# Kernel tuning notes

Hardware: AMD Instinct MI355X
Metric: run time of the kernel (lower is better)

## Reference

```python
import jax, jax.numpy as jnp
import numpy as np

N_EMBD = 2048
HEAD_SIZE = 128

def setup_inputs() -> dict:
    key = jax.random.key(0)
    kx, kk, kq, kv = jax.random.split(key, 4)
    bound = 1.0 / np.sqrt(N_EMBD)  # torch Linear default init range
    x = jax.random.normal(kx, (4, 4096, N_EMBD), dtype=jnp.float32)
    Wk = jax.random.uniform(kk, (N_EMBD, HEAD_SIZE), jnp.float32, -bound, bound)
    Wq = jax.random.uniform(kq, (N_EMBD, HEAD_SIZE), jnp.float32, -bound, bound)
    Wv = jax.random.uniform(kv, (N_EMBD, HEAD_SIZE), jnp.float32, -bound, bound)
    return {"x": x, "Wk": Wk, "Wq": Wq, "Wv": Wv}

def reference(x, Wk, Wq, Wv):
    B, T, C = x.shape
    k = jnp.einsum('btc,ch->bth', x, Wk)
    q = jnp.einsum('btc,ch->bth', x, Wq)
    v = jnp.einsum('btc,ch->bth', x, Wv)
    # NOTE: original scales by C**-0.5 where C = n_embd (input dim), not head_size
    scores = jnp.einsum('bth,bsh->bts', q, k) * (C ** -0.5)
    causal = jnp.tril(jnp.ones((T, T), dtype=bool))  # [T,T]
    scores = jnp.where(causal, scores, -jnp.inf)
    probs = jax.nn.softmax(scores, axis=-1)
    # dropout_probability = 0.0 -> identity
    return jnp.einsum('bts,bsh->bth', probs, v)
```

## Files before the change

kernel.cpp:

```cpp
#include <hip/hip_runtime.h>
#include <hip/hip_bf16.h>

#define T_SEQ 4096
#define NB 4
#define CEMB 2048
#define HS 128

typedef __attribute__((ext_vector_type(8))) short bf16x8;
typedef __attribute__((ext_vector_type(4))) float f32x4;
typedef __attribute__((ext_vector_type(16))) float f32x16;

__device__ inline short f2bf(float f) {
    union { float f; unsigned u; } v; v.f = f;
    unsigned r = v.u + 0x7FFFu + ((v.u >> 16) & 1u);
    return (short)(r >> 16);
}

__device__ inline unsigned pk2(float lo, float hi) {
    unsigned r;
    asm("v_cvt_pk_bf16_f32 %0, %1, %2" : "=v"(r) : "v"(lo), "v"(hi));
    return r;
}

__device__ inline void gld16(const void* gsrc, void* lds) {
    __builtin_amdgcn_global_load_lds(
        (const __attribute__((address_space(1))) unsigned*)gsrc,
        (__attribute__((address_space(3))) unsigned*)lds, 16, 0, 0);
}

__global__ __launch_bounds__(256) void wt_kernel(
    const float* __restrict__ Wq, const float* __restrict__ Wk,
    const float* __restrict__ Wv, short* __restrict__ Wt) {
    int d = blockIdx.x * 256 + threadIdx.x;
    int mat = d >> 18;
    int rm  = d & 262143;
    int s   = rm >> 13;
    int e   = rm & 8191;
    int p   = e * 2;
    int n   = p >> 7;
    int lin = p ^ ((n & 7) << 4);
    int kk  = (lin & 127) >> 1;
    int k   = s * 64 + kk;
    const float* W = (mat == 0) ? Wq : (mat == 1) ? Wk : Wv;
    Wt[d] = f2bf(W[k * HS + n]);
}

__global__ __launch_bounds__(256, 3) void proj_kernel(
    const float* __restrict__ x, const short* __restrict__ Wt,
    short* __restrict__ qg, short* __restrict__ kg, short* __restrict__ vtg) {
    __shared__ short Wlds[3][8192];

    const int tid = threadIdx.x;
    const int w   = tid >> 6;
    const int l   = tid & 63;
    const int lg  = l >> 4;
    const int lr  = l & 15;

    const int bid = blockIdx.x;
    const int wk  = (bid & 7) * 96 + (bid >> 3);
    const int mat = wk % 3;
    const int m0  = (wk / 3) * 64;

    const short* Wp = Wt + (long)mat * 262144;

    f32x4 acc[8];
    #pragma unroll
    for (int b = 0; b < 8; b++) acc[b] = (f32x4){0.f, 0.f, 0.f, 0.f};

    const float* xrow = x + (long)(m0 + w * 16 + lr) * CEMB;
    const int sw = (lr & 7) << 4;

    float4 xs[3][4];

#define STAGE(S, B) do {                                                   \
        const short* gp_ = Wp + (long)(S) * 8192 + (long)(w * 4) * 512 + l * 8; \
        gld16(gp_,        &Wlds[B][(w * 4 + 0) * 512]);                    \
        gld16(gp_ + 512,  &Wlds[B][(w * 4 + 1) * 512]);                    \
        gld16(gp_ + 1024, &Wlds[B][(w * 4 + 2) * 512]);                    \
        gld16(gp_ + 1536, &Wlds[B][(w * 4 + 3) * 512]);                    \
    } while (0)

#define LOADX(S, B) do {                                                   \
        const float* xn_ = xrow + (S) * 64;                                \
        xs[B][0] = *reinterpret_cast<const float4*>(xn_ + lg * 8);         \
        xs[B][1] = *reinterpret_cast<const float4*>(xn_ + lg * 8 + 4);     \
        xs[B][2] = *reinterpret_cast<const float4*>(xn_ + 32 + lg * 8);    \
        xs[B][3] = *reinterpret_cast<const float4*>(xn_ + 32 + lg * 8 + 4);\
    } while (0)

    STAGE(0, 0);
    LOADX(0, 0);
    STAGE(1, 1);
    LOADX(1, 1);

#define STEP(S, B0, B2) do {                                               \
        asm volatile("s_waitcnt vmcnt(8) lgkmcnt(0)\n\ts_barrier" ::: "memory"); \
        if ((S) + 2 < 32) { STAGE((S) + 2, B2); LOADX((S) + 2, B2); }      \
        bf16x8 a0, a1;                                                     \
        a0[0] = f2bf(xs[B0][0].x); a0[1] = f2bf(xs[B0][0].y);              \
        a0[2] = f2bf(xs[B0][0].z); a0[3] = f2bf(xs[B0][0].w);              \
        a0[4] = f2bf(xs[B0][1].x); a0[5] = f2bf(xs[B0][1].y);              \
        a0[6] = f2bf(xs[B0][1].z); a0[7] = f2bf(xs[B0][1].w);              \
        a1[0] = f2bf(xs[B0][2].x); a1[1] = f2bf(xs[B0][2].y);              \
        a1[2] = f2bf(xs[B0][2].z); a1[3] = f2bf(xs[B0][2].w);              \
        a1[4] = f2bf(xs[B0][3].x); a1[5] = f2bf(xs[B0][3].y);              \
        a1[6] = f2bf(xs[B0][3].z); a1[7] = f2bf(xs[B0][3].w);              \
        const char* lbase_ = (const char*)&Wlds[B0][0];                    \
        _Pragma("unroll")                                                  \
        for (int nt = 0; nt < 8; nt++) {                                   \
            int off_ = (((nt * 16 + lr) * 128 + lg * 16)) ^ sw;            \
            bf16x8 bfr_ = *reinterpret_cast<const bf16x8*>(lbase_ + off_); \
            acc[nt] = __builtin_amdgcn_mfma_f32_16x16x32_bf16(             \
                a0, bfr_, acc[nt], 0, 0, 0);                               \
        }                                                                  \
        _Pragma("unroll")                                                  \
        for (int nt = 0; nt < 8; nt++) {                                   \
            int off_ = (((nt * 16 + lr) * 128 + lg * 16 + 64)) ^ sw;       \
            bf16x8 bfr_ = *reinterpret_cast<const bf16x8*>(lbase_ + off_); \
            acc[nt] = __builtin_amdgcn_mfma_f32_16x16x32_bf16(             \
                a1, bfr_, acc[nt], 0, 0, 0);                               \
        }                                                                  \
    } while (0)

    for (int s = 0; s < 30; s += 3) {
        STEP(s, 0, 2);
        STEP(s + 1, 1, 0);
        STEP(s + 2, 2, 1);
    }
    STEP(30, 0, 2);
    STEP(31, 1, 0);

#undef STEP
#undef LOADX
#undef STAGE

    if (mat == 0) {
        const float scale = 0.0318793851f;
        #pragma unroll
        for (int nt = 0; nt < 8; nt++)
            #pragma unroll
            for (int r = 0; r < 4; r++) {
                int row = m0 + w * 16 + lg * 4 + r;
                qg[(long)row * HS + nt * 16 + lr] = f2bf(acc[nt][r] * scale);
            }
    } else if (mat == 1) {
        short* kt = kg + ((long)(m0 >> 6)) * 8192;
        #pragma unroll
        for (int nt = 0; nt < 8; nt++)
            #pragma unroll
            for (int r = 0; r < 4; r++) {
                int r64  = w * 16 + lg * 4 + r;
                int byte = (r64 * 256 + (nt * 16 + lr) * 2) ^ ((r64 & 7) << 4);
                kt[byte >> 1] = f2bf(acc[nt][r]);
            }
    } else {
        #pragma unroll
        for (int nt = 0; nt < 8; nt++)
            #pragma unroll
            for (int r = 0; r < 4; r++) {
                int row = m0 + w * 16 + lg * 4 + r;
                int b   = row >> 12;
                int tl  = row & 4095;
                vtg[(long)b * (HS * T_SEQ) + (long)(nt * 16 + lr) * T_SEQ + tl]
                    = f2bf(acc[nt][r]);
            }
    }
}

__global__ __launch_bounds__(512, 2) void attn_kernel(
    const short* __restrict__ qg, const short* __restrict__ kg,
    const short* __restrict__ vtg, float* __restrict__ out) {
    __shared__ __align__(16) char pool[131072];
    __shared__ float Lm[8][32];
    __shared__ float Ll[8][32];

    const int tid = threadIdx.x;
    const int w   = tid >> 6;
    const int l   = tid & 63;
    const int c31 = l & 31;
    const int hi  = l >> 5;
    const int hi4 = hi << 2;
    const int hi8 = hi << 3;

    const int bid = blockIdx.x;
    const int xcd = bid & 7;
    const int idx = bid >> 3;
    const int b   = xcd >> 1;
    const int qtA = 127 - ((idx << 1) | (xcd & 1));

    const short* kbimg = kg + (long)b * 64 * 8192;
    const short* vb    = vtg + (long)b * HS * T_SEQ;

    short* Kw = (short*)(pool + (w << 14));

#define STAGEK(TILE) do {                                                  \
        const short* gp_ = kbimg + (long)(TILE) * 8192 + l * 8;            \
        _Pragma("unroll")                                                  \
        for (int i = 0; i < 16; i++)                                       \
            gld16(gp_ + i * 512, Kw + i * 512 + l * 8);                    \
    } while (0)

    const int swz = (c31 & 7) << 4;
    const int rbA = c31 * 256;
    const int rbB = (32 + c31) * 256;

    #pragma unroll 1
    for (int ph = 0; ph < 2; ++ph) {
        const int qt   = ph ? (127 - qtA) : qtA;
        const int q0   = qt * 32;
        const int qrow = q0 + c31;
        const int ntk  = (qt >> 1) + 1;

        bf16x8 qf[8];
        #pragma unroll
        for (int kc = 0; kc < 8; kc++)
            qf[kc] = *reinterpret_cast<const bf16x8*>(
                &qg[(long)(b * T_SEQ + qrow) * HS + kc * 16 + hi8]);

        f32x16 accO[4];
        #pragma unroll
        for (int nb = 0; nb < 4; nb++)
            #pragma unroll
            for (int i = 0; i < 16; i++) accO[nb][i] = 0.f;
        float mrow = -__builtin_inff();
        float lsum = 0.f;

        if (w < ntk) STAGEK(w);

        #pragma unroll 1
        for (int t = w; t < ntk; t += 8) {
            const int kv0 = t * 64;

            asm volatile("s_waitcnt vmcnt(0)" ::: "memory");

            bf16x8 vfA[2][4];
            #pragma unroll
            for (int kc = 0; kc < 2; kc++)
                #pragma unroll
                for (int nb = 0; nb < 4; nb++)
                    vfA[kc][nb] = *reinterpret_cast<const bf16x8*>(
                        &vb[(long)(nb * 32 + c31) * T_SEQ + kv0 + kc * 16 + hi8]);

            f32x16 SA, SB;
            #pragma unroll
            for (int i = 0; i < 16; i++) { SA[i] = 0.f; SB[i] = 0.f; }
            __builtin_amdgcn_s_setprio(1);
            #pragma unroll
            for (int kc = 0; kc < 8; kc++) {
                const int cb = kc * 32 + hi * 16;
                bf16x8 ka = *reinterpret_cast<const bf16x8*>(
                    (const char*)Kw + ((rbA + cb) ^ swz));
                bf16x8 kb2 = *reinterpret_cast<const bf16x8*>(
                    (const char*)Kw + ((rbB + cb) ^ swz));
                SA = __builtin_amdgcn_mfma_f32_32x32x16_bf16(ka,  qf[kc], SA, 0, 0, 0);
                SB = __builtin_amdgcn_mfma_f32_32x32x16_bf16(kb2, qf[kc], SB, 0, 0, 0);
            }
            __builtin_amdgcn_s_setprio(0);

            if (t + 8 < ntk) STAGEK(t + 8);

            float pA[16], pB[16];
            #pragma unroll
            for (int r = 0; r < 16; r++) { pA[r] = SA[r]; pB[r] = SB[r]; }

            if (kv0 + 63 > q0) {
                #pragma unroll
                for (int r = 0; r < 16; r++) {
                    int kr = kv0 + (r & 3) + 8 * (r >> 2) + hi4;
                    pA[r] = (kr > qrow)      ? -__builtin_inff() : pA[r];
                    pB[r] = (kr + 32 > qrow) ? -__builtin_inff() : pB[r];
                }
            }

            float t16[16];
            #pragma unroll
            for (int r = 0; r < 16; r++) t16[r] = fmaxf(pA[r], pB[r]);
            #pragma unroll
            for (int s2 = 8; s2 >= 1; s2 >>= 1)
                #pragma unroll
                for (int r = 0; r < 8; r++)
                    if (r < s2) t16[r] = fmaxf(t16[r], t16[r + s2]);
            float mt = fmaxf(t16[0], __shfl_xor(t16[0], 32));

            if (__any(mt > mrow)) {
                float mnew = fmaxf(mrow, mt);
                float fac  = exp2f(mrow - mnew);
                lsum *= fac;
                #pragma unroll
                for (int nb = 0; nb < 4; nb++)
                    #pragma unroll
                    for (int i = 0; i < 16; i++) accO[nb][i] *= fac;
                mrow = mnew;
            }

            bf16x8 vfB[2][4];
            #pragma unroll
            for (int kc = 0; kc < 2; kc++)
                #pragma unroll
                for (int nb = 0; nb < 4; nb++)
                    vfB[kc][nb] = *reinterpret_cast<const bf16x8*>(
                        &vb[(long)(nb * 32 + c31) * T_SEQ + kv0 + (kc + 2) * 16 + hi8]);

            #pragma unroll
            for (int r = 0; r < 16; r++) {
                pA[r] = exp2f(pA[r] - mrow);
                pB[r] = exp2f(pB[r] - mrow);
            }
            float s16[16];
            #pragma unroll
            for (int r = 0; r < 16; r++) s16[r] = pA[r] + pB[r];
            #pragma unroll
            for (int s2 = 8; s2 >= 1; s2 >>= 1)
                #pragma unroll
                for (int r = 0; r < 8; r++)
                    if (r < s2) s16[r] += s16[r + s2];
            lsum += s16[0] + __shfl_xor(s16[0], 32);

            bf16x8 pf[4];
            #pragma unroll
            for (int kc = 0; kc < 4; kc++) {
                const int V0 = 2 * kc, V1 = 2 * kc + 1;
                const int r0 = ((V0 >> 2) << 4) | ((V0 & 3) << 2);
                const int r1 = ((V1 >> 2) << 4) | ((V1 & 3) << 2);
#define PSEL(i) ((i) < 16 ? pA[(i) & 15] : pB[(i) & 15])
                unsigned a0 = pk2(PSEL(r0 + 0), PSEL(r0 + 1));
                unsigned a1 = pk2(PSEL(r0 + 2), PSEL(r0 + 3));
                unsigned b0 = pk2(PSEL(r1 + 0), PSEL(r1 + 1));
                unsigned b1 = pk2(PSEL(r1 + 2), PSEL(r1 + 3));
#undef PSEL
                unsigned k0 = hi ? b0 : a0, k1 = hi ? b1 : a1;
                unsigned s0 = hi ? a0 : b0, s1 = hi ? a1 : b1;
                unsigned g0 = (unsigned)__shfl_xor((int)s0, 32);
                unsigned g1 = (unsigned)__shfl_xor((int)s1, 32);
                union { unsigned u[4]; bf16x8 v; } U;
                U.u[0] = hi ? g0 : k0;
                U.u[1] = hi ? g1 : k1;
                U.u[2] = hi ? k0 : g0;
                U.u[3] = hi ? k1 : g1;
                pf[kc] = U.v;
            }

            __builtin_amdgcn_s_setprio(1);
            #pragma unroll
            for (int nb = 0; nb < 4; nb++)
                accO[nb] = __builtin_amdgcn_mfma_f32_32x32x16_bf16(pf[0], vfA[0][nb], accO[nb], 0, 0, 0);
            #pragma unroll
            for (int nb = 0; nb < 4; nb++)
                accO[nb] = __builtin_amdgcn_mfma_f32_32x32x16_bf16(pf[1], vfA[1][nb], accO[nb], 0, 0, 0);
            #pragma unroll
            for (int nb = 0; nb < 4; nb++)
                accO[nb] = __builtin_amdgcn_mfma_f32_32x32x16_bf16(pf[2], vfB[0][nb], accO[nb], 0, 0, 0);
            #pragma unroll
            for (int nb = 0; nb < 4; nb++)
                accO[nb] = __builtin_amdgcn_mfma_f32_32x32x16_bf16(pf[3], vfB[1][nb], accO[nb], 0, 0, 0);
            __builtin_amdgcn_s_setprio(0);
        }

        __syncthreads();
        {
            float* LaccW = (float*)(pool + (w << 14));
            #pragma unroll
            for (int nb = 0; nb < 4; nb++)
                #pragma unroll
                for (int r = 0; r < 16; r++)
                    LaccW[((r & 3) + 8 * (r >> 2) + hi4) * 128 + nb * 32 + c31] = accO[nb][r];
            if (l < 32) { Lm[w][c31] = mrow; Ll[w][c31] = lsum; }
        }
        __syncthreads();

        {
            const int row = tid >> 4;
            const int c0  = (tid & 15) * 8;
            float mv[8], lv[8];
            #pragma unroll
            for (int p2 = 0; p2 < 8; p2++) { mv[p2] = Lm[p2][row]; lv[p2] = Ll[p2][row]; }
            float ms = mv[0];
            #pragma unroll
            for (int p2 = 1; p2 < 8; p2++) ms = fmaxf(ms, mv[p2]);
            float fv[8];
            float L = 0.f;
            #pragma unroll
            for (int p2 = 0; p2 < 8; p2++) { fv[p2] = exp2f(mv[p2] - ms); L += lv[p2] * fv[p2]; }
            float inv = 1.0f / L;
            float* op = &out[((long)b * T_SEQ + q0 + row) * HS + c0];
            #pragma unroll
            for (int j = 0; j < 8; j++) {
                float o = 0.f;
                #pragma unroll
                for (int p2 = 0; p2 < 8; p2++)
                    o += ((const float*)(pool + (p2 << 14)))[row * 128 + c0 + j] * fv[p2];
                op[j] = o * inv;
            }
        }
        __syncthreads();
    }
#undef STAGEK
}

extern "C" void kernel_launch(void* const* d_in, const int* in_sizes, int n_in,
                              void* d_out, int out_size, void* d_ws, size_t ws_size,
                              hipStream_t stream) {
    const float* x  = (const float*)d_in[0];
    const float* Wk = (const float*)d_in[1];
    const float* Wq = (const float*)d_in[2];
    const float* Wv = (const float*)d_in[3];
    float* out = (float*)d_out;

    char* ws = (char*)d_ws;
    short* Wt  = (short*)ws;
    short* qg  = (short*)(ws + 1572864);
    short* kg  = (short*)(ws + 1572864 + 4194304);
    short* vtg = (short*)(ws + 1572864 + 8388608);

    wt_kernel  <<<3072, 256, 0, stream>>>(Wq, Wk, Wv, Wt);
    proj_kernel<<<768,  256, 0, stream>>>(x, Wt, qg, kg, vtg);
    attn_kernel<<<256,  512, 0, stream>>>(qg, kg, vtg, out);
}
```

Baseline: 133.5 us.

## Double projection block rows to 128 with 8 waves sharing each weight stage

The projection kernel now uses 512-thread blocks that each cover 128 rows instead of 64, so every weight tile staged in LDS serves twice as many rows and weight traffic per row is halved. The x prefetch becomes single-buffered: x is converted to bf16 right after the barrier and the next slice is loaded immediately, which cuts register use (launch bounds now ask for 6 waves per SIMD). The key-tile store indexing is adjusted for the larger block. In exchange, the loop is no longer unrolled, x load latency is hidden behind only one step of MFMA work, and there are half as many blocks to fill the CUs.

```diff
diff --git a/kernel.cpp b/kernel.cpp
--- a/kernel.cpp
+++ b/kernel.cpp
@@ -45,7 +45,7 @@
     Wt[d] = f2bf(W[k * HS + n]);
 }
 
-__global__ __launch_bounds__(256, 3) void proj_kernel(
+__global__ __launch_bounds__(512, 6) void proj_kernel(
     const float* __restrict__ x, const short* __restrict__ Wt,
     short* __restrict__ qg, short* __restrict__ kg, short* __restrict__ vtg) {
     __shared__ short Wlds[3][8192];
@@ -57,9 +57,9 @@
     const int lr  = l & 15;
 
     const int bid = blockIdx.x;
-    const int wk  = (bid & 7) * 96 + (bid >> 3);
+    const int wk  = (bid & 7) * 48 + (bid >> 3);
     const int mat = wk % 3;
-    const int m0  = (wk / 3) * 64;
+    const int m0  = (wk / 3) * 128;
 
     const short* Wp = Wt + (long)mat * 262144;
 
@@ -70,67 +70,74 @@
     const float* xrow = x + (long)(m0 + w * 16 + lr) * CEMB;
     const int sw = (lr & 7) << 4;
 
-    float4 xs[3][4];
+    float4 xs0, xs1, xs2, xs3;
 
 #define STAGE(S, B) do {                                                   \
-        const short* gp_ = Wp + (long)(S) * 8192 + (long)(w * 4) * 512 + l * 8; \
-        gld16(gp_,        &Wlds[B][(w * 4 + 0) * 512]);                    \
-        gld16(gp_ + 512,  &Wlds[B][(w * 4 + 1) * 512]);                    \
-        gld16(gp_ + 1024, &Wlds[B][(w * 4 + 2) * 512]);                    \
-        gld16(gp_ + 1536, &Wlds[B][(w * 4 + 3) * 512]);                    \
+        const short* gp_ = Wp + (long)(S) * 8192 + (long)(w * 2) * 512 + l * 8; \
+        gld16(gp_,       &Wlds[B][(w * 2 + 0) * 512]);                     \
+        gld16(gp_ + 512, &Wlds[B][(w * 2 + 1) * 512]);                     \
     } while (0)
 
-#define LOADX(S, B) do {                                                   \
+#define LOADX(S) do {                                                      \
         const float* xn_ = xrow + (S) * 64;                                \
-        xs[B][0] = *reinterpret_cast<const float4*>(xn_ + lg * 8);         \
-        xs[B][1] = *reinterpret_cast<const float4*>(xn_ + lg * 8 + 4);     \
-        xs[B][2] = *reinterpret_cast<const float4*>(xn_ + 32 + lg * 8);    \
-        xs[B][3] = *reinterpret_cast<const float4*>(xn_ + 32 + lg * 8 + 4);\
+        xs0 = *reinterpret_cast<const float4*>(xn_ + lg * 8);              \
+        xs1 = *reinterpret_cast<const float4*>(xn_ + lg * 8 + 4);          \
+        xs2 = *reinterpret_cast<const float4*>(xn_ + 32 + lg * 8);         \
+        xs3 = *reinterpret_cast<const float4*>(xn_ + 32 + lg * 8 + 4);     \
     } while (0)
 
-    STAGE(0, 0);
-    LOADX(0, 0);
-    STAGE(1, 1);
-    LOADX(1, 1);
-
-#define STEP(S, B0, B2) do {                                               \
-        asm volatile("s_waitcnt vmcnt(8) lgkmcnt(0)\n\ts_barrier" ::: "memory"); \
-        if ((S) + 2 < 32) { STAGE((S) + 2, B2); LOADX((S) + 2, B2); }      \
-        bf16x8 a0, a1;                                                     \
-        a0[0] = f2bf(xs[B0][0].x); a0[1] = f2bf(xs[B0][0].y);              \
-        a0[2] = f2bf(xs[B0][0].z); a0[3] = f2bf(xs[B0][0].w);              \
-        a0[4] = f2bf(xs[B0][1].x); a0[5] = f2bf(xs[B0][1].y);              \
-        a0[6] = f2bf(xs[B0][1].z); a0[7] = f2bf(xs[B0][1].w);              \
-        a1[0] = f2bf(xs[B0][2].x); a1[1] = f2bf(xs[B0][2].y);              \
-        a1[2] = f2bf(xs[B0][2].z); a1[3] = f2bf(xs[B0][2].w);              \
-        a1[4] = f2bf(xs[B0][3].x); a1[5] = f2bf(xs[B0][3].y);              \
-        a1[6] = f2bf(xs[B0][3].z); a1[7] = f2bf(xs[B0][3].w);              \
-        const char* lbase_ = (const char*)&Wlds[B0][0];                    \
+#define CONVERT(A0, A1) do {                                               \
+        A0[0] = f2bf(xs0.x); A0[1] = f2bf(xs0.y);                          \
+        A0[2] = f2bf(xs0.z); A0[3] = f2bf(xs0.w);                          \
+        A0[4] = f2bf(xs1.x); A0[5] = f2bf(xs1.y);                          \
+        A0[6] = f2bf(xs1.z); A0[7] = f2bf(xs1.w);                          \
+        A1[0] = f2bf(xs2.x); A1[1] = f2bf(xs2.y);                          \
+        A1[2] = f2bf(xs2.z); A1[3] = f2bf(xs2.w);                          \
+        A1[4] = f2bf(xs3.x); A1[5] = f2bf(xs3.y);                          \
+        A1[6] = f2bf(xs3.z); A1[7] = f2bf(xs3.w);                          \
+    } while (0)
+
+#define MFMA16(LB) do {                                                    \
         _Pragma("unroll")                                                  \
         for (int nt = 0; nt < 8; nt++) {                                   \
             int off_ = (((nt * 16 + lr) * 128 + lg * 16)) ^ sw;            \
-            bf16x8 bfr_ = *reinterpret_cast<const bf16x8*>(lbase_ + off_); \
+            bf16x8 bfr_ = *reinterpret_cast<const bf16x8*>((LB) + off_);   \
             acc[nt] = __builtin_amdgcn_mfma_f32_16x16x32_bf16(             \
                 a0, bfr_, acc[nt], 0, 0, 0);                               \
         }                                                                  \
         _Pragma("unroll")                                                  \
         for (int nt = 0; nt < 8; nt++) {                                   \
             int off_ = (((nt * 16 + lr) * 128 + lg * 16 + 64)) ^ sw;       \
-            bf16x8 bfr_ = *reinterpret_cast<const bf16x8*>(lbase_ + off_); \
+            bf16x8 bfr_ = *reinterpret_cast<const bf16x8*>((LB) + off_);   \
             acc[nt] = __builtin_amdgcn_mfma_f32_16x16x32_bf16(             \
                 a1, bfr_, acc[nt], 0, 0, 0);                               \
         }                                                                  \
     } while (0)
 
-    for (int s = 0; s < 30; s += 3) {
-        STEP(s, 0, 2);
-        STEP(s + 1, 1, 0);
-        STEP(s + 2, 2, 1);
+    LOADX(0);
+    STAGE(0, 0);
+    STAGE(1, 1);
+
+    #pragma unroll 1
+    for (int s = 0; s < 31; ++s) {
+        asm volatile("s_waitcnt vmcnt(2) lgkmcnt(0)\n\ts_barrier" ::: "memory");
+        bf16x8 a0, a1;
+        CONVERT(a0, a1);
+        LOADX(s + 1);
+        if (s + 2 < 32) STAGE(s + 2, (s + 2) % 3);
+        const char* lbase_ = (const char*)&Wlds[s % 3][0];
+        MFMA16(lbase_);
     }
-    STEP(30, 0, 2);
-    STEP(31, 1, 0);
-
-#undef STEP
+    {
+        asm volatile("s_waitcnt vmcnt(0) lgkmcnt(0)\n\ts_barrier" ::: "memory");
+        bf16x8 a0, a1;
+        CONVERT(a0, a1);
+        const char* lbase_ = (const char*)&Wlds[31 % 3][0];
+        MFMA16(lbase_);
+    }
+
+#undef MFMA16
+#undef CONVERT
 #undef LOADX
 #undef STAGE
 
@@ -144,14 +151,15 @@
                 qg[(long)row * HS + nt * 16 + lr] = f2bf(acc[nt][r] * scale);
             }
     } else if (mat == 1) {
-        short* kt = kg + ((long)(m0 >> 6)) * 8192;
         #pragma unroll
         for (int nt = 0; nt < 8; nt++)
             #pragma unroll
             for (int r = 0; r < 4; r++) {
-                int r64  = w * 16 + lg * 4 + r;
+                int gr   = w * 16 + lg * 4 + r;
+                long tile = (m0 >> 6) + (gr >> 6);
+                int r64  = gr & 63;
                 int byte = (r64 * 256 + (nt * 16 + lr) * 2) ^ ((r64 & 7) << 4);
-                kt[byte >> 1] = f2bf(acc[nt][r]);
+                kg[tile * 8192 + (byte >> 1)] = f2bf(acc[nt][r]);
             }
     } else {
         #pragma unroll
@@ -413,6 +421,6 @@
     short* vtg = (short*)(ws + 1572864 + 8388608);
 
     wt_kernel  <<<3072, 256, 0, stream>>>(Wq, Wk, Wv, Wt);
-    proj_kernel<<<768,  256, 0, stream>>>(x, Wt, qg, kg, vtg);
+    proj_kernel<<<384,  512, 0, stream>>>(x, Wt, qg, kg, vtg);
     attn_kernel<<<256,  512, 0, stream>>>(qg, kg, vtg, out);
 }
```

After: 169.3 us. +26.9%, slower.

## Rewrite projection GEMM with 32x32 MFMA and direct fragment-layout weight loads

Applied to the files above, without the earlier changes.

The projection kernel drops its LDS-staged, barrier-synchronised triple-buffered weight pipeline. Weights are now pre-permuted into the per-lane fragment layout of 32x32x16 MFMA and read straight from global/L2 into registers, and x rows are software-prefetched one step ahead. Each wave computes a 32x64 tile instead of 16x128, and bf16 conversion uses the packed cvt instruction. This removes LDS traffic and block barriers, at the cost of more global weight reads per wave that rely on cache hits.

```diff
diff --git a/kernel.cpp b/kernel.cpp
--- a/kernel.cpp
+++ b/kernel.cpp
@@ -31,139 +31,113 @@
 __global__ __launch_bounds__(256) void wt_kernel(
     const float* __restrict__ Wq, const float* __restrict__ Wk,
     const float* __restrict__ Wv, short* __restrict__ Wt) {
-    int d = blockIdx.x * 256 + threadIdx.x;
-    int mat = d >> 18;
-    int rm  = d & 262143;
-    int s   = rm >> 13;
-    int e   = rm & 8191;
-    int p   = e * 2;
-    int n   = p >> 7;
-    int lin = p ^ ((n & 7) << 4);
-    int kk  = (lin & 127) >> 1;
-    int k   = s * 64 + kk;
+    int idx = blockIdx.x * 256 + threadIdx.x;
+    int j    = idx & 7;
+    int lane = (idx >> 3) & 63;
+    int c32  = (idx >> 9) & 3;
+    int k16  = (idx >> 11) & 127;
+    int mat  = idx >> 18;
+    int col  = c32 * 32 + (lane & 31);
+    int k    = k16 * 16 + ((lane >> 5) << 3) + j;
     const float* W = (mat == 0) ? Wq : (mat == 1) ? Wk : Wv;
-    Wt[d] = f2bf(W[k * HS + n]);
+    Wt[idx] = f2bf(W[k * HS + col]);
 }
 
 __global__ __launch_bounds__(256, 3) void proj_kernel(
     const float* __restrict__ x, const short* __restrict__ Wt,
     short* __restrict__ qg, short* __restrict__ kg, short* __restrict__ vtg) {
-    __shared__ short Wlds[3][8192];
-
     const int tid = threadIdx.x;
     const int w   = tid >> 6;
     const int l   = tid & 63;
-    const int lg  = l >> 4;
-    const int lr  = l & 15;
+    const int c31 = l & 31;
+    const int hi  = l >> 5;
 
     const int bid = blockIdx.x;
     const int wk  = (bid & 7) * 96 + (bid >> 3);
     const int mat = wk % 3;
     const int m0  = (wk / 3) * 64;
 
-    const short* Wp = Wt + (long)mat * 262144;
-
-    f32x4 acc[8];
+    const int rgbase = (w >> 1) << 5;
+    const int wc     = (w & 1) << 6;
+    const int c32b   = wc >> 5;
+
+    const short* Wm = Wt + (long)mat * 262144;
+    const float* xrow = x + (long)(m0 + rgbase + c31) * CEMB + hi * 8;
+
+    f32x16 acc0, acc1;
     #pragma unroll
-    for (int b = 0; b < 8; b++) acc[b] = (f32x4){0.f, 0.f, 0.f, 0.f};
-
-    const float* xrow = x + (long)(m0 + w * 16 + lr) * CEMB;
-    const int sw = (lr & 7) << 4;
-
-    float4 xs[3][4];
-
-#define STAGE(S, B) do {                                                   \
-        const short* gp_ = Wp + (long)(S) * 8192 + (long)(w * 4) * 512 + l * 8; \
-        gld16(gp_,        &Wlds[B][(w * 4 + 0) * 512]);                    \
-        gld16(gp_ + 512,  &Wlds[B][(w * 4 + 1) * 512]);                    \
-        gld16(gp_ + 1024, &Wlds[B][(w * 4 + 2) * 512]);                    \
-        gld16(gp_ + 1536, &Wlds[B][(w * 4 + 3) * 512]);                    \
-    } while (0)
-
-#define LOADX(S, B) do {                                                   \
-        const float* xn_ = xrow + (S) * 64;                                \
-        xs[B][0] = *reinterpret_cast<const float4*>(xn_ + lg * 8);         \
-        xs[B][1] = *reinterpret_cast<const float4*>(xn_ + lg * 8 + 4);     \
-        xs[B][2] = *reinterpret_cast<const float4*>(xn_ + 32 + lg * 8);    \
-        xs[B][3] = *reinterpret_cast<const float4*>(xn_ + 32 + lg * 8 + 4);\
-    } while (0)
-
-    STAGE(0, 0);
-    LOADX(0, 0);
-    STAGE(1, 1);
-    LOADX(1, 1);
-
-#define STEP(S, B0, B2) do {                                               \
-        asm volatile("s_waitcnt vmcnt(8) lgkmcnt(0)\n\ts_barrier" ::: "memory"); \
-        if ((S) + 2 < 32) { STAGE((S) + 2, B2); LOADX((S) + 2, B2); }      \
-        bf16x8 a0, a1;                                                     \
-        a0[0] = f2bf(xs[B0][0].x); a0[1] = f2bf(xs[B0][0].y);              \
-        a0[2] = f2bf(xs[B0][0].z); a0[3] = f2bf(xs[B0][0].w);              \
-        a0[4] = f2bf(xs[B0][1].x); a0[5] = f2bf(xs[B0][1].y);              \
-        a0[6] = f2bf(xs[B0][1].z); a0[7] = f2bf(xs[B0][1].w);              \
-        a1[0] = f2bf(xs[B0][2].x); a1[1] = f2bf(xs[B0][2].y);              \
-        a1[2] = f2bf(xs[B0][2].z); a1[3] = f2bf(xs[B0][2].w);              \
-        a1[4] = f2bf(xs[B0][3].x); a1[5] = f2bf(xs[B0][3].y);              \
-        a1[6] = f2bf(xs[B0][3].z); a1[7] = f2bf(xs[B0][3].w);              \
-        const char* lbase_ = (const char*)&Wlds[B0][0];                    \
-        _Pragma("unroll")                                                  \
-        for (int nt = 0; nt < 8; nt++) {                                   \
-            int off_ = (((nt * 16 + lr) * 128 + lg * 16)) ^ sw;            \
-            bf16x8 bfr_ = *reinterpret_cast<const bf16x8*>(lbase_ + off_); \
-            acc[nt] = __builtin_amdgcn_mfma_f32_16x16x32_bf16(             \
-                a0, bfr_, acc[nt], 0, 0, 0);                               \
-        }                                                                  \
-        _Pragma("unroll")                                                  \
-        for (int nt = 0; nt < 8; nt++) {                                   \
-            int off_ = (((nt * 16 + lr) * 128 + lg * 16 + 64)) ^ sw;       \
-            bf16x8 bfr_ = *reinterpret_cast<const bf16x8*>(lbase_ + off_); \
-            acc[nt] = __builtin_amdgcn_mfma_f32_16x16x32_bf16(             \
-                a1, bfr_, acc[nt], 0, 0, 0);                               \
-        }                                                                  \
-    } while (0)
-
-    for (int s = 0; s < 30; s += 3) {
-        STEP(s, 0, 2);
-        STEP(s + 1, 1, 0);
-        STEP(s + 2, 2, 1);
+    for (int i = 0; i < 16; i++) { acc0[i] = 0.f; acc1[i] = 0.f; }
+
+    float4 xc[4][2], xn[4][2];
+    #pragma unroll
+    for (int kc = 0; kc < 4; kc++) {
+        xc[kc][0] = *reinterpret_cast<const float4*>(xrow + kc * 16);
+        xc[kc][1] = *reinterpret_cast<const float4*>(xrow + kc * 16 + 4);
     }
-    STEP(30, 0, 2);
-    STEP(31, 1, 0);
-
-#undef STEP
-#undef LOADX
-#undef STAGE
+
+    #pragma unroll 2
+    for (int s = 0; s < 32; ++s) {
+        if (s < 31) {
+            const float* xp = xrow + (s + 1) * 64;
+            #pragma unroll
+            for (int kc = 0; kc < 4; kc++) {
+                xn[kc][0] = *reinterpret_cast<const float4*>(xp + kc * 16);
+                xn[kc][1] = *reinterpret_cast<const float4*>(xp + kc * 16 + 4);
+            }
+        }
+
+        #pragma unroll
+        for (int kc = 0; kc < 4; kc++) {
+            union { unsigned u[4]; bf16x8 v; } A;
+            A.u[0] = pk2(xc[kc][0].x, xc[kc][0].y);
+            A.u[1] = pk2(xc[kc][0].z, xc[kc][0].w);
+            A.u[2] = pk2(xc[kc][1].x, xc[kc][1].y);
+            A.u[3] = pk2(xc[kc][1].z, xc[kc][1].w);
+
+            const long k16 = (long)(s * 4 + kc);
+            bf16x8 w0 = *reinterpret_cast<const bf16x8*>(
+                Wm + (k16 * 4 + c32b) * 512 + l * 8);
+            bf16x8 w1 = *reinterpret_cast<const bf16x8*>(
+                Wm + (k16 * 4 + c32b + 1) * 512 + l * 8);
+
+            acc0 = __builtin_amdgcn_mfma_f32_32x32x16_bf16(A.v, w0, acc0, 0, 0, 0);
+            acc1 = __builtin_amdgcn_mfma_f32_32x32x16_bf16(A.v, w1, acc1, 0, 0, 0);
+        }
+
+        #pragma unroll
+        for (int kc = 0; kc < 4; kc++) { xc[kc][0] = xn[kc][0]; xc[kc][1] = xn[kc][1]; }
+    }
 
     if (mat == 0) {
         const float scale = 0.0318793851f;
         #pragma unroll
-        for (int nt = 0; nt < 8; nt++)
-            #pragma unroll
-            for (int r = 0; r < 4; r++) {
-                int row = m0 + w * 16 + lg * 4 + r;
-                qg[(long)row * HS + nt * 16 + lr] = f2bf(acc[nt][r] * scale);
-            }
+        for (int r = 0; r < 16; r++) {
+            int grow = m0 + rgbase + (r & 3) + 8 * (r >> 2) + 4 * hi;
+            qg[(long)grow * HS + wc + c31]      = f2bf(acc0[r] * scale);
+            qg[(long)grow * HS + wc + 32 + c31] = f2bf(acc1[r] * scale);
+        }
     } else if (mat == 1) {
-        short* kt = kg + ((long)(m0 >> 6)) * 8192;
-        #pragma unroll
-        for (int nt = 0; nt < 8; nt++)
-            #pragma unroll
-            for (int r = 0; r < 4; r++) {
-                int r64  = w * 16 + lg * 4 + r;
-                int byte = (r64 * 256 + (nt * 16 + lr) * 2) ^ ((r64 & 7) << 4);
-                kt[byte >> 1] = f2bf(acc[nt][r]);
-            }
+        #pragma unroll
+        for (int r = 0; r < 16; r++) {
+            int grow = m0 + rgbase + (r & 3) + 8 * (r >> 2) + 4 * hi;
+            long tile = grow >> 6;
+            int r64  = grow & 63;
+            int d0   = wc + c31;
+            int b0   = (r64 * 256 + d0 * 2) ^ ((r64 & 7) << 4);
+            int b1   = (r64 * 256 + (d0 + 32) * 2) ^ ((r64 & 7) << 4);
+            kg[tile * 8192 + (b0 >> 1)] = f2bf(acc0[r]);
+            kg[tile * 8192 + (b1 >> 1)] = f2bf(acc1[r]);
+        }
     } else {
         #pragma unroll
-        for (int nt = 0; nt < 8; nt++)
-            #pragma unroll
-            for (int r = 0; r < 4; r++) {
-                int row = m0 + w * 16 + lg * 4 + r;
-                int b   = row >> 12;
-                int tl  = row & 4095;
-                vtg[(long)b * (HS * T_SEQ) + (long)(nt * 16 + lr) * T_SEQ + tl]
-                    = f2bf(acc[nt][r]);
-            }
+        for (int r = 0; r < 16; r++) {
+            int grow = m0 + rgbase + (r & 3) + 8 * (r >> 2) + 4 * hi;
+            int b2 = grow >> 12;
+            int tl = grow & 4095;
+            int d0 = wc + c31;
+            vtg[(long)b2 * (HS * T_SEQ) + (long)d0 * T_SEQ + tl]        = f2bf(acc0[r]);
+            vtg[(long)b2 * (HS * T_SEQ) + (long)(d0 + 32) * T_SEQ + tl] = f2bf(acc1[r]);
+        }
     }
 }
 
```

Result: slower. 181.3 us (+35.8%).

## Repartition projection GEMM so each wave owns private W columns without barriers

Applied to the files above, without the earlier changes.

The projection kernel now gives each wave a private 32-column slice of the weight tile across all 64 rows, instead of splitting rows across waves that share the whole weight tile. Each wave then reads only its own LDS region, so the per-step workgroup barrier is removed and LDS shrinks to a double buffer. The weight pre-layout kernel is rewritten to match, and x-to-bf16 conversion switches to the packed hardware convert. The trade-off is that every wave now loads x for all 64 rows, which quadruples x global traffic per block, and the K-step is halved so there are twice as many iterations.

```diff
diff --git a/kernel.cpp b/kernel.cpp
--- a/kernel.cpp
+++ b/kernel.cpp
@@ -32,23 +32,22 @@
     const float* __restrict__ Wq, const float* __restrict__ Wk,
     const float* __restrict__ Wv, short* __restrict__ Wt) {
     int d = blockIdx.x * 256 + threadIdx.x;
+    int j   = d & 7;
+    int l   = (d >> 3) & 63;
+    int ct  = (d >> 9) & 1;
+    int wq  = (d >> 10) & 3;
+    int s2  = (d >> 12) & 63;
     int mat = d >> 18;
-    int rm  = d & 262143;
-    int s   = rm >> 13;
-    int e   = rm & 8191;
-    int p   = e * 2;
-    int n   = p >> 7;
-    int lin = p ^ ((n & 7) << 4);
-    int kk  = (lin & 127) >> 1;
-    int k   = s * 64 + kk;
+    int col = wq * 32 + ct * 16 + (l & 15);
+    int k   = s2 * 32 + ((l >> 4) << 3) + j;
     const float* W = (mat == 0) ? Wq : (mat == 1) ? Wk : Wv;
-    Wt[d] = f2bf(W[k * HS + n]);
+    Wt[d] = f2bf(W[k * HS + col]);
 }
 
 __global__ __launch_bounds__(256, 3) void proj_kernel(
     const float* __restrict__ x, const short* __restrict__ Wt,
     short* __restrict__ qg, short* __restrict__ kg, short* __restrict__ vtg) {
-    __shared__ short Wlds[3][8192];
+    __shared__ short Wlds[2][4][1024];
 
     const int tid = threadIdx.x;
     const int w   = tid >> 6;
@@ -61,74 +60,110 @@
     const int mat = wk % 3;
     const int m0  = (wk / 3) * 64;
 
-    const short* Wp = Wt + (long)mat * 262144;
-
-    f32x4 acc[8];
+    const short* Wp = Wt + (long)mat * 262144 + w * 1024;
+
+    f32x4 acc[4][2];
     #pragma unroll
-    for (int b = 0; b < 8; b++) acc[b] = (f32x4){0.f, 0.f, 0.f, 0.f};
-
-    const float* xrow = x + (long)(m0 + w * 16 + lr) * CEMB;
-    const int sw = (lr & 7) << 4;
-
-    float4 xs[3][4];
-
-#define STAGE(S, B) do {                                                   \
-        const short* gp_ = Wp + (long)(S) * 8192 + (long)(w * 4) * 512 + l * 8; \
-        gld16(gp_,        &Wlds[B][(w * 4 + 0) * 512]);                    \
-        gld16(gp_ + 512,  &Wlds[B][(w * 4 + 1) * 512]);                    \
-        gld16(gp_ + 1024, &Wlds[B][(w * 4 + 2) * 512]);                    \
-        gld16(gp_ + 1536, &Wlds[B][(w * 4 + 3) * 512]);                    \
+    for (int a = 0; a < 4; a++)
+        #pragma unroll
+        for (int b = 0; b < 2; b++) acc[a][b] = (f32x4){0.f, 0.f, 0.f, 0.f};
+
+    const float* xr0 = x + (long)(m0 + 0 * 16 + lr) * CEMB + lg * 8;
+    const float* xr1 = x + (long)(m0 + 1 * 16 + lr) * CEMB + lg * 8;
+    const float* xr2 = x + (long)(m0 + 2 * 16 + lr) * CEMB + lg * 8;
+    const float* xr3 = x + (long)(m0 + 3 * 16 + lr) * CEMB + lg * 8;
+
+    float4 xs[2][8];
+
+#define STAGE(S2, B) do {                                                  \
+        const short* gp_ = Wp + (long)(S2) * 4096 + l * 8;                 \
+        gld16(gp_,       &Wlds[B][w][0]);                                  \
+        gld16(gp_ + 512, &Wlds[B][w][512]);                                \
     } while (0)
 
-#define LOADX(S, B) do {                                                   \
-        const float* xn_ = xrow + (S) * 64;                                \
-        xs[B][0] = *reinterpret_cast<const float4*>(xn_ + lg * 8);         \
-        xs[B][1] = *reinterpret_cast<const float4*>(xn_ + lg * 8 + 4);     \
-        xs[B][2] = *reinterpret_cast<const float4*>(xn_ + 32 + lg * 8);    \
-        xs[B][3] = *reinterpret_cast<const float4*>(xn_ + 32 + lg * 8 + 4);\
+#define LOADX(S2, XB) do {                                                 \
+        xs[XB][0] = *reinterpret_cast<const float4*>(xr0 + (S2) * 32);     \
+        xs[XB][1] = *reinterpret_cast<const float4*>(xr0 + (S2) * 32 + 4); \
+        xs[XB][2] = *reinterpret_cast<const float4*>(xr1 + (S2) * 32);     \
+        xs[XB][3] = *reinterpret_cast<const float4*>(xr1 + (S2) * 32 + 4); \
+        xs[XB][4] = *reinterpret_cast<const float4*>(xr2 + (S2) * 32);     \
+        xs[XB][5] = *reinterpret_cast<const float4*>(xr2 + (S2) * 32 + 4); \
+        xs[XB][6] = *reinterpret_cast<const float4*>(xr3 + (S2) * 32);     \
+        xs[XB][7] = *reinterpret_cast<const float4*>(xr3 + (S2) * 32 + 4); \
     } while (0)
 
+#define STEP(S2) do {                                                      \
+        asm volatile("s_waitcnt vmcnt(8)" ::: "memory");                   \
+        if ((S2) + 1 < 64) {                                               \
+            STAGE((S2) + 1, ((S2) + 1) & 1);                               \
+            __builtin_amdgcn_sched_barrier(0);         \
+        }                                                                  \
+        const char* lb_ = (const char*)&Wlds[(S2) & 1][w][0] + l * 16;     \
+        bf16x8 b0_ = *reinterpret_cast<const bf16x8*>(lb_);                \
+        bf16x8 b1_ = *reinterpret_cast<const bf16x8*>(lb_ + 1024);        \
+        bf16x8 A0_, A1_, A2_, A3_;                                         \
+        {                                                                  \
+            union { unsigned u[4]; bf16x8 v; } U_;                         \
+            U_.u[0] = pk2(xs[(S2) & 1][0].x, xs[(S2) & 1][0].y);           \
+            U_.u[1] = pk2(xs[(S2) & 1][0].z, xs[(S2) & 1][0].w);           \
+            U_.u[2] = pk2(xs[(S2) & 1][1].x, xs[(S2) & 1][1].y);           \
+            U_.u[3] = pk2(xs[(S2) & 1][1].z, xs[(S2) & 1][1].w);           \
+            A0_ = U_.v;                                                    \
+            U_.u[0] = pk2(xs[(S2) & 1][2].x, xs[(S2) & 1][2].y);           \
+            U_.u[1] = pk2(xs[(S2) & 1][2].z, xs[(S2) & 1][2].w);           \
+            U_.u[2] = pk2(xs[(S2) & 1][3].x, xs[(S2) & 1][3].y);           \
+            U_.u[3] = pk2(xs[(S2) & 1][3].z, xs[(S2) & 1][3].w);           \
+            A1_ = U_.v;                                                    \
+            U_.u[0] = pk2(xs[(S2) & 1][4].x, xs[(S2) & 1][4].y);           \
+            U_.u[1] = pk2(xs[(S2) & 1][4].z, xs[(S2) & 1][4].w);           \
+            U_.u[2] = pk2(xs[(S2) & 1][5].x, xs[(S2) & 1][5].y);           \
+            U_.u[3] = pk2(xs[(S2) & 1][5].z, xs[(S2) & 1][5].w);           \
+            A2_ = U_.v;                                                    \
+            U_.u[0] = pk2(xs[(S2) & 1][6].x, xs[(S2) & 1][6].y);           \
+            U_.u[1] = pk2(xs[(S2) & 1][6].z, xs[(S2) & 1][6].w);           \
+            U_.u[2] = pk2(xs[(S2) & 1][7].x, xs[(S2) & 1][7].y);           \
+            U_.u[3] = pk2(xs[(S2) & 1][7].z, xs[(S2) & 1][7].w);           \
+            A3_ = U_.v;                                                    \
+        }                                                                  \
+        if ((S2) + 2 < 64) LOADX((S2) + 2, (S2) & 1);                      \
+        acc[0][0] = __builtin_amdgcn_mfma_f32_16x16x32_bf16(A0_, b0_, acc[0][0], 0, 0, 0); \
+        acc[0][1] = __builtin_amdgcn_mfma_f32_16x16x32_bf16(A0_, b1_, acc[0][1], 0, 0, 0); \
+        acc[1][0] = __builtin_amdgcn_mfma_f32_16x16x32_bf16(A1_, b0_, acc[1][0], 0, 0, 0); \
+        acc[1][1] = __builtin_amdgcn_mfma_f32_16x16x32_bf16(A1_, b1_, acc[1][1], 0, 0, 0); \
+        acc[2][0] = __builtin_amdgcn_mfma_f32_16x16x32_bf16(A2_, b0_, acc[2][0], 0, 0, 0); \
+        acc[2][1] = __builtin_amdgcn_mfma_f32_16x16x32_bf16(A2_, b1_, acc[2][1], 0, 0, 0); \
+        acc[3][0] = __builtin_amdgcn_mfma_f32_16x16x32_bf16(A3_, b0_, acc[3][0], 0, 0, 0); \
+        acc[3][1] = __builtin_amdgcn_mfma_f32_16x16x32_bf16(A3_, b1_, acc[3][1], 0, 0, 0); \
+    } while (0)
+
     STAGE(0, 0);
+    __builtin_amdgcn_sched_barrier(0);
     LOADX(0, 0);
-    STAGE(1, 1);
     LOADX(1, 1);
 
-#define STEP(S, B0, B2) do {                                               \
-        asm volatile("s_waitcnt vmcnt(8) lgkmcnt(0)\n\ts_barrier" ::: "memory"); \
-        if ((S) + 2 < 32) { STAGE((S) + 2, B2); LOADX((S) + 2, B2); }      \
-        bf16x8 a0, a1;                                                     \
-        a0[0] = f2bf(xs[B0][0].x); a0[1] = f2bf(xs[B0][0].y);              \
-        a0[2] = f2bf(xs[B0][0].z); a0[3] = f2bf(xs[B0][0].w);              \
-        a0[4] = f2bf(xs[B0][1].x); a0[5] = f2bf(xs[B0][1].y);              \
-        a0[6] = f2bf(xs[B0][1].z); a0[7] = f2bf(xs[B0][1].w);              \
-        a1[0] = f2bf(xs[B0][2].x); a1[1] = f2bf(xs[B0][2].y);              \
-        a1[2] = f2bf(xs[B0][2].z); a1[3] = f2bf(xs[B0][2].w);              \
-        a1[4] = f2bf(xs[B0][3].x); a1[5] = f2bf(xs[B0][3].y);              \
-        a1[6] = f2bf(xs[B0][3].z); a1[7] = f2bf(xs[B0][3].w);              \
-        const char* lbase_ = (const char*)&Wlds[B0][0];                    \
-        _Pragma("unroll")                                                  \
-        for (int nt = 0; nt < 8; nt++) {                                   \
-            int off_ = (((nt * 16 + lr) * 128 + lg * 16)) ^ sw;            \
-            bf16x8 bfr_ = *reinterpret_cast<const bf16x8*>(lbase_ + off_); \
-            acc[nt] = __builtin_amdgcn_mfma_f32_16x16x32_bf16(             \
-                a0, bfr_, acc[nt], 0, 0, 0);                               \
-        }                                                                  \
-        _Pragma("unroll")                                                  \
-        for (int nt = 0; nt < 8; nt++) {                                   \
-            int off_ = (((nt * 16 + lr) * 128 + lg * 16 + 64)) ^ sw;       \
-            bf16x8 bfr_ = *reinterpret_cast<const bf16x8*>(lbase_ + off_); \
-            acc[nt] = __builtin_amdgcn_mfma_f32_16x16x32_bf16(             \
-                a1, bfr_, acc[nt], 0, 0, 0);                               \
-        }                                                                  \
-    } while (0)
-
-    for (int s = 0; s < 30; s += 3) {
-        STEP(s, 0, 2);
-        STEP(s + 1, 1, 0);
-        STEP(s + 2, 2, 1);
+    #pragma unroll
+    for (int s2 = 0; s2 < 63; ++s2) STEP(s2);
+    {
+        asm volatile("s_waitcnt vmcnt(0)" ::: "memory");
+        const char* lb_ = (const char*)&Wlds[63 & 1][w][0] + l * 16;
+        bf16x8 b0_ = *reinterpret_cast<const bf16x8*>(lb_);
+        bf16x8 b1_ = *reinterpret_cast<const bf16x8*>(lb_ + 1024);
+        union { unsigned u[4]; bf16x8 v; } U_;
+        bf16x8 A_[4];
+        #pragma unroll
+        for (int rgp = 0; rgp < 4; rgp++) {
+            U_.u[0] = pk2(xs[1][rgp * 2].x, xs[1][rgp * 2].y);
+            U_.u[1] = pk2(xs[1][rgp * 2].z, xs[1][rgp * 2].w);
+            U_.u[2] = pk2(xs[1][rgp * 2 + 1].x, xs[1][rgp * 2 + 1].y);
+            U_.u[3] = pk2(xs[1][rgp * 2 + 1].z, xs[1][rgp * 2 + 1].w);
+            A_[rgp] = U_.v;
+        }
+        #pragma unroll
+        for (int rgp = 0; rgp < 4; rgp++) {
+            acc[rgp][0] = __builtin_amdgcn_mfma_f32_16x16x32_bf16(A_[rgp], b0_, acc[rgp][0], 0, 0, 0);
+            acc[rgp][1] = __builtin_amdgcn_mfma_f32_16x16x32_bf16(A_[rgp], b1_, acc[rgp][1], 0, 0, 0);
+        }
     }
-    STEP(30, 0, 2);
-    STEP(31, 1, 0);
 
 #undef STEP
 #undef LOADX
@@ -137,33 +172,42 @@
     if (mat == 0) {
         const float scale = 0.0318793851f;
         #pragma unroll
-        for (int nt = 0; nt < 8; nt++)
-            #pragma unroll
-            for (int r = 0; r < 4; r++) {
-                int row = m0 + w * 16 + lg * 4 + r;
-                qg[(long)row * HS + nt * 16 + lr] = f2bf(acc[nt][r] * scale);
-            }
+        for (int rgp = 0; rgp < 4; rgp++)
+            #pragma unroll
+            for (int ct = 0; ct < 2; ct++)
+                #pragma unroll
+                for (int r = 0; r < 4; r++) {
+                    int row = m0 + rgp * 16 + lg * 4 + r;
+                    int col = w * 32 + ct * 16 + lr;
+                    qg[(long)row * HS + col] = f2bf(acc[rgp][ct][r] * scale);
+                }
     } else if (mat == 1) {
         short* kt = kg + ((long)(m0 >> 6)) * 8192;
         #pragma unroll
-        for (int nt = 0; nt < 8; nt++)
-            #pragma unroll
-            for (int r = 0; r < 4; r++) {
-                int r64  = w * 16 + lg * 4 + r;
-                int byte = (r64 * 256 + (nt * 16 + lr) * 2) ^ ((r64 & 7) << 4);
-                kt[byte >> 1] = f2bf(acc[nt][r]);
-            }
+        for (int rgp = 0; rgp < 4; rgp++)
+            #pragma unroll
+            for (int ct = 0; ct < 2; ct++)
+                #pragma unroll
+                for (int r = 0; r < 4; r++) {
+                    int r64  = rgp * 16 + lg * 4 + r;
+                    int d0   = w * 32 + ct * 16 + lr;
+                    int byte = (r64 * 256 + d0 * 2) ^ ((r64 & 7) << 4);
+                    kt[byte >> 1] = f2bf(acc[rgp][ct][r]);
+                }
     } else {
         #pragma unroll
-        for (int nt = 0; nt < 8; nt++)
-            #pragma unroll
-            for (int r = 0; r < 4; r++) {
-                int row = m0 + w * 16 + lg * 4 + r;
-                int b   = row >> 12;
-                int tl  = row & 4095;
-                vtg[(long)b * (HS * T_SEQ) + (long)(nt * 16 + lr) * T_SEQ + tl]
-                    = f2bf(acc[nt][r]);
-            }
+        for (int rgp = 0; rgp < 4; rgp++)
+            #pragma unroll
+            for (int ct = 0; ct < 2; ct++)
+                #pragma unroll
+                for (int r = 0; r < 4; r++) {
+                    int row = m0 + rgp * 16 + lg * 4 + r;
+                    int b2  = row >> 12;
+                    int tl  = row & 4095;
+                    int d0  = w * 32 + ct * 16 + lr;
+                    vtg[(long)b2 * (HS * T_SEQ) + (long)d0 * T_SEQ + tl]
+                        = f2bf(acc[rgp][ct][r]);
+                }
     }
 }
 
```

Result: slower. 252.0 us (+88.8%).
